# Kernel tuning notes

Hardware: AMD Instinct MI355X
Metric: run time of the kernel (lower is better)

## Reference

```python
import jax, jax.numpy as jnp
import numpy as np

N_P, N_W, F_IN = 512, 3584, 256
H1, O1 = 8, 32
H2, O2 = 8, 256
BATCH = 1024
NEG_SLOPE = 0.2


def _xavier(key, shape):
    fan_in, fan_out = shape[-2], shape[-1]
    lim = jnp.sqrt(6.0 / (fan_in + fan_out))
    return jax.random.uniform(key, shape, jnp.float32, -lim, lim)


def setup_inputs() -> dict:
    key = jax.random.key(0)
    ks = jax.random.split(key, 16)
    return {
        "input": jax.random.uniform(ks[0], (BATCH, N_W), jnp.float32),
        "pern_feature": jax.random.normal(ks[1], (N_P, F_IN), jnp.float32),
        "word_feature": jax.random.normal(ks[2], (N_W, F_IN), jnp.float32),
        "w1": _xavier(ks[3], (H1, F_IN, O1)),
        "a_src1": _xavier(ks[4], (H1, O1, 1)),
        "a_dst1": _xavier(ks[5], (H1, O1, 1)),
        "b1": jnp.zeros((O1,), jnp.float32),
        "w2": _xavier(ks[6], (H2, F_IN, O2)),
        "a_src2": _xavier(ks[7], (H2, F_IN, 1)),
        "a_dst2": _xavier(ks[8], (H2, F_IN, 1)),
        "b2": jnp.zeros((O2,), jnp.float32),
        "W_fc": _xavier(ks[9], (O2, 5)),
        "b_fc": jnp.zeros((5,), jnp.float32),
        "pern_adj": jax.random.randint(ks[10], (N_P, N_P), 0, 2, jnp.int32),
        "word_pern_adj": jax.random.randint(ks[11], (N_P + N_W, N_P + N_W), 0, 2, jnp.int32),
    }


def gat(h, adj, w, a_src, a_dst, bias):
    # h: [N, f_in], adj: [N, N] int, w: [H, f_in, f_out]
    h_prime = jnp.einsum('nf,hfo->hno', h, w)          # [H, N, O]
    t = jnp.tanh(h_prime)
    s_src = jnp.einsum('hno,hoi->hn', t, a_src)        # [H, N]
    s_dst = jnp.einsum('hno,hoi->hn', t, a_dst)        # [H, N]
    attn = s_src[:, :, None] + s_dst[:, None, :]       # [H, N, N]
    attn = jnp.where(attn >= 0, attn, NEG_SLOPE * attn)  # leaky_relu
    attn = jnp.where(adj[None, :, :] > 0, attn, -jnp.inf)
    attn = jax.nn.softmax(attn, axis=-1)
    out = jnp.einsum('hnm,hmo->hno', attn, h_prime)    # [H, N, O]
    return out + bias


def reference(input, pern_feature, word_feature, w1, a_src1, a_dst1, b1,
              w2, a_src2, a_dst2, b2, W_fc, b_fc, pern_adj, word_pern_adj):
    n_p = pern_feature.shape[0]
    # GAT 1 over personality graph
    h1 = gat(pern_feature, pern_adj, w1, a_src1, a_dst1, b1)       # [H1, n_p, O1]
    hiddn_pp = jnp.transpose(h1, (1, 0, 2)).reshape(n_p, -1)        # [n_p, H1*O1]
    hiddn_pp = jax.nn.elu(hiddn_pp)
    # dropout is identity in eval mode
    hiddn_wp = jnp.concatenate([word_feature, hiddn_pp], axis=0)    # [N, 256]
    h2 = gat(hiddn_wp, word_pern_adj, w2, a_src2, a_dst2, b2)       # [H2, N, O2]
    hiddn_wp2 = h2.mean(axis=0)                                     # [N, O2]
    hiddn_w = hiddn_wp2[:word_feature.shape[0], :]                  # [n_w, O2]
    x = (input @ hiddn_w) / input.sum(axis=1, keepdims=True)        # [B, O2]
    return x @ W_fc + b_fc                                          # [B, 5]
```

## Files before the change

kernel.cpp:

```cpp
#include <hip/hip_runtime.h>
#include <hip/hip_bf16.h>
#include <math.h>

#define NP 512
#define NW 3584
#define NT 4096
#define FIN 256
#define H1 8
#define O1 32
#define H2 8
#define O2 256
#define NEG 0.2f

typedef __attribute__((ext_vector_type(8))) short bf16x8;
typedef __attribute__((ext_vector_type(4))) float f32x4;
typedef unsigned long long u64;

__device__ __forceinline__ unsigned short f2bf(float f) {
    unsigned u = __float_as_uint(f);
    unsigned r = (u + 0x7FFF + ((u >> 16) & 1)) >> 16;
    return (unsigned short)r;
}
__device__ __forceinline__ float rflf(float x) {
    return __uint_as_float(__builtin_amdgcn_readfirstlane(__float_as_uint(x)));
}

__global__ __launch_bounds__(256) void k_prep(
    const float* __restrict__ wf, const float* __restrict__ pf,
    const float* __restrict__ w1, const float* __restrict__ a_src1,
    const float* __restrict__ a_dst1, const float* __restrict__ w2,
    const float* __restrict__ b2, const float* __restrict__ W_fc,
    const float* __restrict__ a_src2, const float* __restrict__ a_dst2,
    const int* __restrict__ wp_adj,
    unsigned short* __restrict__ abf, unsigned short* __restrict__ btbf,
    float* __restrict__ hp1, float* __restrict__ ss1, float* __restrict__ sd1,
    unsigned* __restrict__ maskT, float* __restrict__ cvec,
    float* __restrict__ wtab)
{
    __shared__ float tile[64][65];
    __shared__ float feat[2][FIN];
    __shared__ float red[4][5];
    int blk = blockIdx.x;
    int t = threadIdx.x;
    if (blk < 896) {
        int idx4 = blk * 256 + t;
        float4 x = ((const float4*)wf)[idx4];
        ushort4 y;
        y.x = f2bf(x.x); y.y = f2bf(x.y); y.z = f2bf(x.z); y.w = f2bf(x.w);
        ((ushort4*)abf)[idx4] = y;
    } else if (blk < 1152) {
        int n0 = (blk - 896) * 2;
        feat[0][t] = pf[n0 * FIN + t];
        feat[1][t] = pf[(n0 + 1) * FIN + t];
        __syncthreads();
        int h = t >> 5, o = t & 31;
        float acc0 = 0.f, acc1 = 0.f;
        const float* wcol = w1 + h * FIN * O1 + o;
        #pragma unroll 4
        for (int f = 0; f < FIN; f++) {
            float w = wcol[f * O1];
            acc0 += feat[0][f] * w;
            acc1 += feat[1][f] * w;
        }
        hp1[n0 * 256 + t] = acc0;
        hp1[(n0 + 1) * 256 + t] = acc1;
        float as = a_src1[h * O1 + o];
        float ad = a_dst1[h * O1 + o];
        float accs[2] = {acc0, acc1};
        #pragma unroll
        for (int i = 0; i < 2; i++) {
            float th = tanhf(accs[i]);
            float vs = th * as, vd = th * ad;
            #pragma unroll
            for (int off = 1; off < 32; off <<= 1) {
                vs += __shfl_xor(vs, off);
                vd += __shfl_xor(vd, off);
            }
            if (o == 0) { ss1[h * NP + n0 + i] = vs; sd1[h * NP + n0 + i] = vd; }
        }
    } else if (blk < 1280) {
        int blk2 = blk - 1152;
        int h = blk2 >> 4;
        int f0 = ((blk2 >> 2) & 3) * 64;
        int o0 = (blk2 & 3) * 64;
        #pragma unroll
        for (int rr = 0; rr < 16; rr++) {
            int f = rr * 4 + (t >> 6);
            int o = t & 63;
            tile[f][o] = w2[((size_t)(h * FIN + f0 + f)) * O2 + o0 + o];
        }
        __syncthreads();
        #pragma unroll
        for (int rr = 0; rr < 16; rr++) {
            int o = rr * 4 + (t >> 6);
            int f = t & 63;
            btbf[((size_t)(h * O2 + o0 + o)) * FIN + f0 + f] = f2bf(tile[f][o]);
        }
    } else if (blk < 2176) {
        int w = t >> 6, l = t & 63;
        int r = (blk - 1280) * 4 + w;
        const int4* row = (const int4*)(wp_adj + (size_t)r * NT);
        for (int c4 = 0; c4 < 16; c4++) {
            int4 x = row[c4 * 64 + l];
            u64 nib = (u64)((x.x != 0 ? 1 : 0) | (x.y != 0 ? 2 : 0) |
                            (x.z != 0 ? 4 : 0) | (x.w != 0 ? 8 : 0));
            u64 v = nib << (4 * (l & 15));
            v |= __shfl_xor(v, 1);
            v |= __shfl_xor(v, 2);
            v |= __shfl_xor(v, 4);
            v |= __shfl_xor(v, 8);
            if ((l & 15) == 0) {
                int qw = c4 * 4 + (l >> 4);
                maskT[(size_t)(2 * qw) * NW + r]     = (unsigned)v;
                maskT[(size_t)(2 * qw + 1) * NW + r] = (unsigned)(v >> 32);
            }
        }
    } else if (blk == 2176) {
        float v[5];
        #pragma unroll
        for (int j = 0; j < 5; j++) v[j] = b2[t] * W_fc[t * 5 + j];
        #pragma unroll
        for (int off = 1; off < 64; off <<= 1)
            #pragma unroll
            for (int j = 0; j < 5; j++) v[j] += __shfl_xor(v[j], off);
        int w = t >> 6, l = t & 63;
        if (l == 0) { for (int j = 0; j < 5; j++) red[w][j] = v[j]; }
        __syncthreads();
        if (t == 0)
            for (int j = 0; j < 5; j++) cvec[j] = red[0][j] + red[1][j] + red[2][j] + red[3][j];
    } else {
        int h = blk - 2177;
        int o = t;
        float* dst = wtab + ((size_t)h * O2 + o) * 8;
        float4 d0 = {a_src2[h * O2 + o], a_dst2[h * O2 + o], W_fc[o * 5], W_fc[o * 5 + 1]};
        float4 d1 = {W_fc[o * 5 + 2], W_fc[o * 5 + 3], W_fc[o * 5 + 4], 0.f};
        *(float4*)dst = d0;
        *(float4*)(dst + 4) = d1;
    }
}

__global__ __launch_bounds__(256) void k_gat1_attn(
    const int* __restrict__ adj, const float* __restrict__ hp1,
    const float* __restrict__ ss1, const float* __restrict__ sd1,
    float* __restrict__ g1acc, float* __restrict__ g1den)
{
    __shared__ float af[256];
    __shared__ float p[8][256];
    __shared__ float den8[8];
    int t = threadIdx.x;
    int b = blockIdx.x;
    int n = b >> 1, mh = b & 1;
    int mbase = mh * 256;
    af[t] = adj[n * NP + mbase + t] > 0 ? 1.0f : 0.0f;
    __syncthreads();
    #pragma unroll
    for (int r = 0; r < 8; r++) {
        int idx = r * 256 + t;
        int h = idx >> 8, m = idx & 255;
        float e = ss1[h * NP + n] + sd1[h * NP + mbase + m];
        e = fmaxf(e, NEG * e);
        p[h][m] = af[m] * __expf(e);
    }
    __syncthreads();
    int w = t >> 6, l = t & 63;
    #pragma unroll
    for (int hh = 0; hh < 2; hh++) {
        int h = w + hh * 4;
        float s = 0;
        #pragma unroll
        for (int k = 0; k < 4; k++) s += p[h][l + 64 * k];
        #pragma unroll
        for (int off = 1; off < 64; off <<= 1) s += __shfl_xor(s, off);
        if (l == 0) den8[h] = s;
    }
    __syncthreads();
    int h = t >> 5;
    float acc0 = 0.f, acc1 = 0.f;
    #pragma unroll 8
    for (int m = 0; m < 256; m += 2) {
        acc0 += p[h][m]     * hp1[(mbase + m) * 256 + t];
        acc1 += p[h][m + 1] * hp1[(mbase + m + 1) * 256 + t];
    }
    g1acc[((size_t)mh * NP + n) * 256 + t] = acc0 + acc1;
    if (t < 8) g1den[((size_t)mh * NP + n) * 8 + t] = den8[t];
}

__global__ __launch_bounds__(256) void k_gemm_hp2(
    const unsigned short* __restrict__ abf, const unsigned short* __restrict__ btbf,
    const float* __restrict__ wtab, const float* __restrict__ g1acc,
    const float* __restrict__ g1den, const float* __restrict__ b1,
    float* __restrict__ gpart)
{
    __shared__ unsigned short As[64][264];
    int b = blockIdx.x;
    int h = b & 7, mt = b >> 3;
    int t = threadIdx.x;
    int w = t >> 6, l = t & 63;
    int m0 = mt * 64;
    if (m0 < NW) {
        int row = t >> 5;
        int col8 = (t & 31) * 8;
        #pragma unroll
        for (int u = 0; u < 8; u++)
            *(bf16x8*)(&As[u * 8 + row][col8]) =
                *(const bf16x8*)(abf + (size_t)(m0 + u * 8 + row) * FIN + col8);
    } else {
        int row = t >> 5;
        int col8 = (t & 31) * 8;
        int hc = col8 >> 5;
        #pragma unroll
        for (int u = 0; u < 8; u++) {
            int n = m0 + u * 8 + row - NW;
            float4 a0 = *(const float4*)(g1acc + (size_t)n * 256 + col8);
            float4 a1 = *(const float4*)(g1acc + (size_t)n * 256 + col8 + 4);
            float4 c0 = *(const float4*)(g1acc + ((size_t)NP + n) * 256 + col8);
            float4 c1 = *(const float4*)(g1acc + ((size_t)NP + n) * 256 + col8 + 4);
            float dn = g1den[(size_t)n * 8 + hc] + g1den[((size_t)NP + n) * 8 + hc];
            float inv = 1.0f / dn;
            float vals[8] = {a0.x + c0.x, a0.y + c0.y, a0.z + c0.z, a0.w + c0.w,
                             a1.x + c1.x, a1.y + c1.y, a1.z + c1.z, a1.w + c1.w};
            unsigned short us[8];
            #pragma unroll
            for (int j = 0; j < 8; j++) {
                float r = vals[j] * inv + b1[(col8 & 31) + j];
                r = r > 0.f ? r : expm1f(r);
                us[j] = f2bf(r);
            }
            *(bf16x8*)(&As[u * 8 + row][col8]) = *(bf16x8*)us;
        }
    }
    __syncthreads();
    int n0 = w * 64;
    int lr = l & 15, lq = l >> 4;
    const unsigned short* bbase = btbf + h * O2 * FIN;
    f32x4 acc[4][4];
    #pragma unroll
    for (int i = 0; i < 4; i++)
        #pragma unroll
        for (int j = 0; j < 4; j++) acc[i][j] = (f32x4){0.f, 0.f, 0.f, 0.f};
    #pragma unroll
    for (int k = 0; k < FIN; k += 32) {
        bf16x8 a[4], bf[4];
        int kc = k + lq * 8;
        #pragma unroll
        for (int j = 0; j < 4; j++)
            bf[j] = *(const bf16x8*)(bbase + (size_t)(n0 + j * 16 + lr) * FIN + kc);
        #pragma unroll
        for (int i = 0; i < 4; i++)
            a[i] = *(const bf16x8*)(&As[i * 16 + lr][kc]);
        #pragma unroll
        for (int i = 0; i < 4; i++)
            #pragma unroll
            for (int j = 0; j < 4; j++)
                acc[i][j] = __builtin_amdgcn_mfma_f32_16x16x32_bf16(bf[j], a[i], acc[i][j], 0, 0, 0);
    }
    const float* wt = wtab + (size_t)h * O2 * 8;
    float* base = gpart + ((size_t)h * 4 + w) * NT * 8;
    #pragma unroll
    for (int i = 0; i < 4; i++) {
        float s[7] = {0,0,0,0,0,0,0};
        #pragma unroll
        for (int j = 0; j < 4; j++) {
            #pragma unroll
            for (int r = 0; r < 4; r++) {
                float x = acc[i][j][r];
                float ex = __expf(2.0f * x);
                float th = 1.0f - 2.0f * __builtin_amdgcn_rcpf(ex + 1.0f);
                const float* wp = wt + (size_t)(n0 + j * 16 + lq * 4 + r) * 8;
                float4 wa = *(const float4*)wp;
                float4 wb = *(const float4*)(wp + 4);
                s[0] += th * wa.x;
                s[1] += th * wa.y;
                s[2] += x * wa.z;
                s[3] += x * wa.w;
                s[4] += x * wb.x;
                s[5] += x * wb.y;
                s[6] += x * wb.z;
            }
        }
        #pragma unroll
        for (int q = 0; q < 7; q++) {
            s[q] += __shfl_xor(s[q], 16);
            s[q] += __shfl_xor(s[q], 32);
        }
        if (lq == 0) {
            int m = m0 + i * 16 + lr;
            float* dst = base + (size_t)m * 8;
            #pragma unroll
            for (int q = 0; q < 7; q++) dst[q] = s[q];
        }
    }
}

__global__ __launch_bounds__(256) void k_comb_hp2(
    const float* __restrict__ gpart,
    float* __restrict__ Etab, float* __restrict__ Eptab, float* __restrict__ T)
{
    int idx = blockIdx.x * 256 + threadIdx.x;
    float s[7] = {0,0,0,0,0,0,0};
    #pragma unroll
    for (int sl = 0; sl < 4; sl++) {
        const float* p = gpart + (((size_t)(idx >> 12) * 4 + sl) * NT + (idx & (NT - 1))) * 8;
        #pragma unroll
        for (int q = 0; q < 7; q++) s[q] += p[q];
    }
    Etab[idx]  = __expf(s[0]);
    Eptab[idx] = __expf(NEG * s[0]);
    float4 t0 = {__expf(s[1]), __expf(NEG * s[1]), 1.0f, s[2]};
    float4 t1 = {s[3], s[4], s[5], s[6]};
    *(float4*)(T + (size_t)idx * 8)     = t0;
    *(float4*)(T + (size_t)idx * 8 + 4) = t1;
}

__global__ __launch_bounds__(256) void k_gat2_attn(
    const unsigned* __restrict__ maskT, const float* __restrict__ Etab,
    const float* __restrict__ Eptab, const float* __restrict__ T,
    float* __restrict__ part)
{
    __shared__ unsigned pw[64 * 64];
    int t = threadIdx.x;
    int w = t >> 6, l = t & 63;
    int b = blockIdx.x;
    int nb = b % 56;
    int h  = (b / 56) & 7;
    int c  = b / 448;
    int rbase = nb * 64;
    #pragma unroll
    for (int u = 0; u < 16; u++) {
        int idx = u * 256 + t;
        int wd = idx >> 6, row = idx & 63;
        pw[idx] = maskT[(size_t)(c * 64 + wd) * NW + rbase + row];
    }
    __syncthreads();
    int n0 = rbase + w * 16;
    float E[16], Ep[16];
    #pragma unroll
    for (int i = 0; i < 16; i++) {
        int r = h * NT + n0 + i;
        E[i]  = rflf(Etab[r]);
        Ep[i] = rflf(Eptab[r]);
    }
    float den[16];
    float num[16][5];
    #pragma unroll
    for (int i = 0; i < 16; i++) {
        den[i] = 0.f;
        #pragma unroll
        for (int j = 0; j < 5; j++) num[i][j] = 0.f;
    }
    const float* Th = T + ((size_t)h * NT + c * 2048) * 8;
    int lsh = l & 31;
    int wdh = l >> 5;
    const unsigned* mb0 = pw + w * 16;
    for (int q = 0; q < 32; q++) {
        const float* tp = Th + (size_t)(q * 64 + l) * 8;
        f32x4 t0 = *(const f32x4*)tp;
        f32x4 t1 = *(const f32x4*)(tp + 4);
        const unsigned* mb = mb0 + (q * 2 + wdh) * 64;
        uint4 ma = *(const uint4*)(mb);
        uint4 mc = *(const uint4*)(mb + 4);
        uint4 me = *(const uint4*)(mb + 8);
        uint4 mg = *(const uint4*)(mb + 12);
        unsigned wv[16] = {ma.x, ma.y, ma.z, ma.w, mc.x, mc.y, mc.z, mc.w,
                           me.x, me.y, me.z, me.w, mg.x, mg.y, mg.z, mg.w};
        #pragma unroll
        for (int i = 0; i < 16; i++) {
            float bm = (float)((wv[i] >> lsh) & 1u);
            float pp = fmaxf(t0.x * E[i], t0.y * Ep[i]) * bm;
            den[i] += pp;
            num[i][0] = fmaf(pp, t0.w, num[i][0]);
            num[i][1] = fmaf(pp, t1.x, num[i][1]);
            num[i][2] = fmaf(pp, t1.y, num[i][2]);
            num[i][3] = fmaf(pp, t1.z, num[i][3]);
            num[i][4] = fmaf(pp, t1.w, num[i][4]);
        }
    }
    #pragma unroll
    for (int i = 0; i < 16; i++) {
        float v[6];
        v[0] = den[i];
        #pragma unroll
        for (int j = 0; j < 5; j++) v[1 + j] = num[i][j];
        #pragma unroll
        for (int off = 1; off < 8; off <<= 1)
            #pragma unroll
            for (int k = 0; k < 6; k++) v[k] += __shfl_xor(v[k], off);
        if ((l & 7) == 0) {
            float* dst = part + ((((size_t)c * NW + n0 + i) * 8 + h) * 8 + (l >> 3)) * 8;
            #pragma unroll
            for (int k = 0; k < 6; k++) dst[k] = v[k];
        }
    }
}

__global__ __launch_bounds__(256) void k_gat2_comb(const float* __restrict__ part,
                                                   float* __restrict__ hf) {
    int idx = blockIdx.x * 256 + threadIdx.x;
    int n = idx >> 3, h = idx & 7;
    float den = 0, num[5] = {0,0,0,0,0};
    #pragma unroll
    for (int cc = 0; cc < 2; cc++) {
        #pragma unroll
        for (int s = 0; s < 8; s++) {
            const float* p = part + ((((size_t)cc * NW + n) * 8 + h) * 8 + s) * 8;
            float4 a = *(const float4*)p;
            float4 bq = *(const float4*)(p + 4);
            den += a.x;
            num[0] += a.y; num[1] += a.z; num[2] += a.w;
            num[3] += bq.x; num[4] += bq.y;
        }
    }
    float inv = 1.0f / (den * 8.0f);
    float v[5];
    #pragma unroll
    for (int j = 0; j < 5; j++) v[j] = num[j] * inv;
    #pragma unroll
    for (int off = 1; off < 8; off <<= 1)
        #pragma unroll
        for (int j = 0; j < 5; j++) v[j] += __shfl_xor(v[j], off);
    if (h == 0) {
        #pragma unroll
        for (int j = 0; j < 5; j++) hf[n * 5 + j] = v[j];
    }
}

__global__ __launch_bounds__(256) void k_final(
    const float* __restrict__ input, const float* __restrict__ hf,
    const float* __restrict__ cvec, const float* __restrict__ b_fc,
    float* __restrict__ out)
{
    int b = blockIdx.x, t = threadIdx.x;
    const float4* row4 = (const float4*)(input + (size_t)b * NW);
    const float4* hf4 = (const float4*)hf;
    float s = 0.f, a[5] = {0.f, 0.f, 0.f, 0.f, 0.f};
    for (int idx = t; idx < NW / 4; idx += 256) {
        float4 x = row4[idx];
        float f[20];
        #pragma unroll
        for (int q = 0; q < 5; q++) *(float4*)(f + 4 * q) = hf4[idx * 5 + q];
        s += x.x + x.y + x.z + x.w;
        #pragma unroll
        for (int j = 0; j < 5; j++)
            a[j] += x.x * f[j] + x.y * f[5 + j] + x.z * f[10 + j] + x.w * f[15 + j];
    }
    #pragma unroll
    for (int off = 1; off < 64; off <<= 1) {
        s += __shfl_xor(s, off);
        #pragma unroll
        for (int j = 0; j < 5; j++) a[j] += __shfl_xor(a[j], off);
    }
    __shared__ float red[4][6];
    int w = t >> 6, l = t & 63;
    if (l == 0) { red[w][0] = s; for (int j = 0; j < 5; j++) red[w][j + 1] = a[j]; }
    __syncthreads();
    if (t < 5) {
        float st = red[0][0] + red[1][0] + red[2][0] + red[3][0];
        float aj = red[0][t + 1] + red[1][t + 1] + red[2][t + 1] + red[3][t + 1];
        out[b * 5 + t] = aj / st + cvec[t] + b_fc[t];
    }
}

extern "C" void kernel_launch(void* const* d_in, const int* in_sizes, int n_in,
                              void* d_out, int out_size, void* d_ws, size_t ws_size,
                              hipStream_t stream) {
    const float* input   = (const float*)d_in[0];
    const float* pf      = (const float*)d_in[1];
    const float* wf      = (const float*)d_in[2];
    const float* w1      = (const float*)d_in[3];
    const float* a_src1  = (const float*)d_in[4];
    const float* a_dst1  = (const float*)d_in[5];
    const float* b1      = (const float*)d_in[6];
    const float* w2      = (const float*)d_in[7];
    const float* a_src2  = (const float*)d_in[8];
    const float* a_dst2  = (const float*)d_in[9];
    const float* b2      = (const float*)d_in[10];
    const float* W_fc    = (const float*)d_in[11];
    const float* b_fc    = (const float*)d_in[12];
    const int* pern_adj  = (const int*)d_in[13];
    const int* wp_adj    = (const int*)d_in[14];
    float* out = (float*)d_out;

    char* ws = (char*)d_ws;
    unsigned short* abf    = (unsigned short*)(ws);
    unsigned short* btbf   = (unsigned short*)(ws + 2097152);
    float*          hp1    = (float*)(ws + 3145728);
    float*          ss1    = (float*)(ws + 3670016);
    float*          sd1    = (float*)(ws + 3686400);
    float*          Etab   = (float*)(ws + 3833856);
    float*          Eptab  = (float*)(ws + 3964928);
    float*          T      = (float*)(ws + 4096000);
    float*          hf     = (float*)(ws + 5144576);
    float*          cvec   = (float*)(ws + 5216256);
    unsigned*       maskT  = (unsigned*)(ws + 5216512);
    float*          gpart  = (float*)(ws + 7051520);
    float*          g1acc  = (float*)(ws + 11245824);
    float*          g1den  = (float*)(ws + 12294400);
    float*          part   = (float*)(ws + 12582912);
    float*          wtab   = (float*)(ws + 28311552);

    k_prep<<<2185, 256, 0, stream>>>(wf, pf, w1, a_src1, a_dst1, w2, b2, W_fc,
                                     a_src2, a_dst2, wp_adj,
                                     abf, btbf, hp1, ss1, sd1, maskT, cvec, wtab);
    k_gat1_attn<<<1024, 256, 0, stream>>>(pern_adj, hp1, ss1, sd1, g1acc, g1den);
    k_gemm_hp2<<<512, 256, 0, stream>>>(abf, btbf, wtab, g1acc, g1den, b1, gpart);
    k_comb_hp2<<<128, 256, 0, stream>>>(gpart, Etab, Eptab, T);
    k_gat2_attn<<<896, 256, 0, stream>>>(maskT, Etab, Eptab, T, part);
    k_gat2_comb<<<112, 256, 0, stream>>>(part, hf);
    k_final<<<1024, 256, 0, stream>>>(input, hf, cvec, b_fc, out);
}
```

Measured before the change: 258.0 us.

## Fuse hp2 partial-sum combine into GEMM and halve row tiles for occupancy

```diff
diff --git a/kernel.cpp b/kernel.cpp
--- a/kernel.cpp
+++ b/kernel.cpp
@@ -189,19 +189,20 @@
     const unsigned short* __restrict__ abf, const unsigned short* __restrict__ btbf,
     const float* __restrict__ wtab, const float* __restrict__ g1acc,
     const float* __restrict__ g1den, const float* __restrict__ b1,
-    float* __restrict__ gpart)
+    float* __restrict__ Etab, float* __restrict__ Eptab, float* __restrict__ T)
 {
-    __shared__ unsigned short As[64][264];
+    __shared__ unsigned short As[32][264];
+    __shared__ float sred[4][32][8];
     int b = blockIdx.x;
     int h = b & 7, mt = b >> 3;
     int t = threadIdx.x;
     int w = t >> 6, l = t & 63;
-    int m0 = mt * 64;
+    int m0 = mt * 32;
     if (m0 < NW) {
         int row = t >> 5;
         int col8 = (t & 31) * 8;
         #pragma unroll
-        for (int u = 0; u < 8; u++)
+        for (int u = 0; u < 4; u++)
             *(bf16x8*)(&As[u * 8 + row][col8]) =
                 *(const bf16x8*)(abf + (size_t)(m0 + u * 8 + row) * FIN + col8);
     } else {
@@ -209,7 +210,7 @@
         int col8 = (t & 31) * 8;
         int hc = col8 >> 5;
         #pragma unroll
-        for (int u = 0; u < 8; u++) {
+        for (int u = 0; u < 4; u++) {
             int n = m0 + u * 8 + row - NW;
             float4 a0 = *(const float4*)(g1acc + (size_t)n * 256 + col8);
             float4 a1 = *(const float4*)(g1acc + (size_t)n * 256 + col8 + 4);
@@ -233,31 +234,30 @@
     int n0 = w * 64;
     int lr = l & 15, lq = l >> 4;
     const unsigned short* bbase = btbf + h * O2 * FIN;
-    f32x4 acc[4][4];
-    #pragma unroll
-    for (int i = 0; i < 4; i++)
+    f32x4 acc[2][4];
+    #pragma unroll
+    for (int i = 0; i < 2; i++)
         #pragma unroll
         for (int j = 0; j < 4; j++) acc[i][j] = (f32x4){0.f, 0.f, 0.f, 0.f};
     #pragma unroll
     for (int k = 0; k < FIN; k += 32) {
-        bf16x8 a[4], bf[4];
+        bf16x8 a[2], bf[4];
         int kc = k + lq * 8;
         #pragma unroll
         for (int j = 0; j < 4; j++)
             bf[j] = *(const bf16x8*)(bbase + (size_t)(n0 + j * 16 + lr) * FIN + kc);
         #pragma unroll
-        for (int i = 0; i < 4; i++)
+        for (int i = 0; i < 2; i++)
             a[i] = *(const bf16x8*)(&As[i * 16 + lr][kc]);
         #pragma unroll
-        for (int i = 0; i < 4; i++)
+        for (int i = 0; i < 2; i++)
             #pragma unroll
             for (int j = 0; j < 4; j++)
                 acc[i][j] = __builtin_amdgcn_mfma_f32_16x16x32_bf16(bf[j], a[i], acc[i][j], 0, 0, 0);
     }
     const float* wt = wtab + (size_t)h * O2 * 8;
-    float* base = gpart + ((size_t)h * 4 + w) * NT * 8;
-    #pragma unroll
-    for (int i = 0; i < 4; i++) {
+    #pragma unroll
+    for (int i = 0; i < 2; i++) {
         float s[7] = {0,0,0,0,0,0,0};
         #pragma unroll
         for (int j = 0; j < 4; j++) {
@@ -284,32 +284,24 @@
             s[q] += __shfl_xor(s[q], 32);
         }
         if (lq == 0) {
-            int m = m0 + i * 16 + lr;
-            float* dst = base + (size_t)m * 8;
-            #pragma unroll
-            for (int q = 0; q < 7; q++) dst[q] = s[q];
-        }
-    }
-}
-
-__global__ __launch_bounds__(256) void k_comb_hp2(
-    const float* __restrict__ gpart,
-    float* __restrict__ Etab, float* __restrict__ Eptab, float* __restrict__ T)
-{
-    int idx = blockIdx.x * 256 + threadIdx.x;
-    float s[7] = {0,0,0,0,0,0,0};
-    #pragma unroll
-    for (int sl = 0; sl < 4; sl++) {
-        const float* p = gpart + (((size_t)(idx >> 12) * 4 + sl) * NT + (idx & (NT - 1))) * 8;
-        #pragma unroll
-        for (int q = 0; q < 7; q++) s[q] += p[q];
-    }
-    Etab[idx]  = __expf(s[0]);
-    Eptab[idx] = __expf(NEG * s[0]);
-    float4 t0 = {__expf(s[1]), __expf(NEG * s[1]), 1.0f, s[2]};
-    float4 t1 = {s[3], s[4], s[5], s[6]};
-    *(float4*)(T + (size_t)idx * 8)     = t0;
-    *(float4*)(T + (size_t)idx * 8 + 4) = t1;
+            #pragma unroll
+            for (int q = 0; q < 7; q++) sred[w][i * 16 + lr][q] = s[q];
+        }
+    }
+    __syncthreads();
+    if (t < 32) {
+        float s[7];
+        #pragma unroll
+        for (int q = 0; q < 7; q++)
+            s[q] = sred[0][t][q] + sred[1][t][q] + sred[2][t][q] + sred[3][t][q];
+        int idx = h * NT + m0 + t;
+        Etab[idx]  = __expf(s[0]);
+        Eptab[idx] = __expf(NEG * s[0]);
+        float4 t0 = {__expf(s[1]), __expf(NEG * s[1]), 1.0f, s[2]};
+        float4 t1 = {s[3], s[4], s[5], s[6]};
+        *(float4*)(T + (size_t)idx * 8)     = t0;
+        *(float4*)(T + (size_t)idx * 8 + 4) = t1;
+    }
 }
 
 __global__ __launch_bounds__(256) void k_gat2_attn(
@@ -317,56 +309,49 @@
     const float* __restrict__ Eptab, const float* __restrict__ T,
     float* __restrict__ part)
 {
-    __shared__ unsigned pw[64 * 64];
+    __shared__ unsigned pw[64 * 32];
     int t = threadIdx.x;
     int w = t >> 6, l = t & 63;
     int b = blockIdx.x;
-    int nb = b % 56;
-    int h  = (b / 56) & 7;
-    int c  = b / 448;
-    int rbase = nb * 64;
-    #pragma unroll
-    for (int u = 0; u < 16; u++) {
+    int nb = b % 112;
+    int h  = (b / 112) & 7;
+    int c  = b / 896;
+    int rbase = nb * 32;
+    #pragma unroll
+    for (int u = 0; u < 8; u++) {
         int idx = u * 256 + t;
-        int wd = idx >> 6, row = idx & 63;
+        int wd = idx >> 5, row = idx & 31;
         pw[idx] = maskT[(size_t)(c * 64 + wd) * NW + rbase + row];
     }
     __syncthreads();
-    int n0 = rbase + w * 16;
-    float E[16], Ep[16];
-    #pragma unroll
-    for (int i = 0; i < 16; i++) {
+    int n0 = rbase + w * 8;
+    float E[8], Ep[8];
+    #pragma unroll
+    for (int i = 0; i < 8; i++) {
         int r = h * NT + n0 + i;
         E[i]  = rflf(Etab[r]);
         Ep[i] = rflf(Eptab[r]);
     }
-    float den[16];
-    float num[16][5];
-    #pragma unroll
-    for (int i = 0; i < 16; i++) {
-        den[i] = 0.f;
-        #pragma unroll
-        for (int j = 0; j < 5; j++) num[i][j] = 0.f;
-    }
+    float den[8] = {0,0,0,0,0,0,0,0};
+    float num[8][5] = {{0}};
     const float* Th = T + ((size_t)h * NT + c * 2048) * 8;
     int lsh = l & 31;
     int wdh = l >> 5;
-    const unsigned* mb0 = pw + w * 16;
+    const unsigned* mbase = pw + w * 8;
     for (int q = 0; q < 32; q++) {
         const float* tp = Th + (size_t)(q * 64 + l) * 8;
         f32x4 t0 = *(const f32x4*)tp;
         f32x4 t1 = *(const f32x4*)(tp + 4);
-        const unsigned* mb = mb0 + (q * 2 + wdh) * 64;
-        uint4 ma = *(const uint4*)(mb);
-        uint4 mc = *(const uint4*)(mb + 4);
-        uint4 me = *(const uint4*)(mb + 8);
-        uint4 mg = *(const uint4*)(mb + 12);
-        unsigned wv[16] = {ma.x, ma.y, ma.z, ma.w, mc.x, mc.y, mc.z, mc.w,
-                           me.x, me.y, me.z, me.w, mg.x, mg.y, mg.z, mg.w};
-        #pragma unroll
-        for (int i = 0; i < 16; i++) {
+        int wd = q * 2 + wdh;
+        uint4 ma = *(const uint4*)(mbase + wd * 32);
+        uint4 mb = *(const uint4*)(mbase + wd * 32 + 4);
+        unsigned wv[8] = {ma.x, ma.y, ma.z, ma.w, mb.x, mb.y, mb.z, mb.w};
+        #pragma unroll
+        for (int i = 0; i < 8; i++) {
             float bm = (float)((wv[i] >> lsh) & 1u);
-            float pp = fmaxf(t0.x * E[i], t0.y * Ep[i]) * bm;
+            float pa = t0.x * E[i];
+            float pb = t0.y * Ep[i];
+            float pp = fmaxf(pa, pb) * bm;
             den[i] += pp;
             num[i][0] = fmaf(pp, t0.w, num[i][0]);
             num[i][1] = fmaf(pp, t1.x, num[i][1]);
@@ -376,7 +361,7 @@
         }
     }
     #pragma unroll
-    for (int i = 0; i < 16; i++) {
+    for (int i = 0; i < 8; i++) {
         float v[6];
         v[0] = den[i];
         #pragma unroll
@@ -492,7 +477,6 @@
     float*          hf     = (float*)(ws + 5144576);
     float*          cvec   = (float*)(ws + 5216256);
     unsigned*       maskT  = (unsigned*)(ws + 5216512);
-    float*          gpart  = (float*)(ws + 7051520);
     float*          g1acc  = (float*)(ws + 11245824);
     float*          g1den  = (float*)(ws + 12294400);
     float*          part   = (float*)(ws + 12582912);
@@ -502,9 +486,9 @@
                                      a_src2, a_dst2, wp_adj,
                                      abf, btbf, hp1, ss1, sd1, maskT, cvec, wtab);
     k_gat1_attn<<<1024, 256, 0, stream>>>(pern_adj, hp1, ss1, sd1, g1acc, g1den);
-    k_gemm_hp2<<<512, 256, 0, stream>>>(abf, btbf, wtab, g1acc, g1den, b1, gpart);
-    k_comb_hp2<<<128, 256, 0, stream>>>(gpart, Etab, Eptab, T);
-    k_gat2_attn<<<896, 256, 0, stream>>>(maskT, Etab, Eptab, T, part);
+    k_gemm_hp2<<<1024, 256, 0, stream>>>(abf, btbf, wtab, g1acc, g1den, b1,
+                                         Etab, Eptab, T);
+    k_gat2_attn<<<1792, 256, 0, stream>>>(maskT, Etab, Eptab, T, part);
     k_gat2_comb<<<112, 256, 0, stream>>>(part, hf);
     k_final<<<1024, 256, 0, stream>>>(input, hf, cvec, b_fc, out);
 }
```

After: 246.6 us. -4.4%, faster.
